# Kernel tuning notes

Measured on AMD Instinct MI355X. Metric: run time of the kernel, lower is better.

## Reference

```python
import jax, jax.numpy as jnp
import numpy as np

N = 50000   # nodes
E = 400000  # edges
D = 128     # hidden = out dim
H = 4       # heads
DH = 32     # head dim (D // H)
T = 3       # node types
R = 6       # relation (edge) types
L = 2       # layers
EPS = 1e-5


def setup_inputs() -> dict:
    key = jax.random.key(0)
    ks = jax.random.split(key, 12)
    s = D ** -0.5
    sh = DH ** -0.5
    return {
        "h": jax.random.normal(ks[0], (N, D), jnp.float32),
        "src": jax.random.randint(ks[1], (E,), 0, N),
        "dst": jax.random.randint(ks[2], (E,), 0, N),
        "ntype": jnp.sort(jax.random.randint(ks[3], (N,), 0, T)),
        "etype": jnp.sort(jax.random.randint(ks[4], (E,), 0, R)),
        # per-layer HGTConv params (stacked over L)
        "Wk": jax.random.normal(ks[5], (L, T, D, D), jnp.float32) * s,
        "Wq": jax.random.normal(ks[6], (L, T, D, D), jnp.float32) * s,
        "Wv": jax.random.normal(ks[7], (L, T, D, D), jnp.float32) * s,
        "Wa": jax.random.normal(ks[8], (L, T, D, D), jnp.float32) * s,
        "W_att": jax.random.normal(ks[9], (L, H, R, DH, DH), jnp.float32) * sh,
        "W_msg": jax.random.normal(ks[10], (L, H, R, DH, DH), jnp.float32) * sh,
        "pri": jnp.ones((L, H, R), jnp.float32),
        "skip": jnp.ones((L, T), jnp.float32),
        "ln_g": jnp.ones((L, D), jnp.float32),
        "ln_b": jnp.zeros((L, D), jnp.float32),
        # LayerAggregator params
        "agg_w": jnp.ones((L,), jnp.float32),
        "agg_g": jnp.ones((D,), jnp.float32),
        "agg_b": jnp.zeros((D,), jnp.float32),
    }


def typed_linear(x, types, W):
    # W: [T, in, out]; per-node-type linear (DGL TypedLinear, no bias)
    out = x @ W[0]
    for t in range(1, W.shape[0]):
        out = jnp.where((types == t)[:, None], x @ W[t], out)
    return out


def edge_typed(x, etype, W):
    # x: [E, H, DH]; W: [H, R, DH, DH]; per-relation, per-head linear
    out = jnp.einsum('ehd,hdo->eho', x, W[:, 0])
    for r in range(1, W.shape[1]):
        out = jnp.where((etype == r)[:, None, None],
                        jnp.einsum('ehd,hdo->eho', x, W[:, r]), out)
    return out


def layer_norm(x, g, b):
    mu = x.mean(-1, keepdims=True)
    var = ((x - mu) ** 2).mean(-1, keepdims=True)
    return (x - mu) * jax.lax.rsqrt(var + EPS) * g + b


def hgt_layer(x, src, dst, ntype, etype, Wk, Wq, Wv, Wa, W_att, W_msg, pri, skip):
    n = x.shape[0]
    k = typed_linear(x, ntype, Wk).reshape(n, H, DH)
    q = typed_linear(x, ntype, Wq).reshape(n, H, DH)
    v = typed_linear(x, ntype, Wv).reshape(n, H, DH)
    kw = edge_typed(k[src], etype, W_att)          # [E,H,DH]
    mv = edge_typed(v[src], etype, W_msg)          # [E,H,DH]
    a = (kw * q[dst]).sum(-1) * pri.T[etype] / np.sqrt(DH).astype(np.float32)  # [E,H]
    # edge softmax over destination nodes
    mx = jax.lax.stop_gradient(jax.ops.segment_max(a, dst, num_segments=n))
    ex = jnp.exp(a - mx[dst])
    den = jax.ops.segment_sum(ex, dst, num_segments=n)
    att = ex / den[dst]                             # [E,H]
    agg = jax.ops.segment_sum(att[:, :, None] * mv, dst, num_segments=n)
    h_a = typed_linear(agg.reshape(n, H * DH), ntype, Wa)
    sk = jax.nn.sigmoid(skip)[ntype][:, None]
    return h_a * sk + x * (1.0 - sk)                # skip gate (dropout = eval identity)


def reference(h, src, dst, ntype, etype, Wk, Wq, Wv, Wa, W_att, W_msg,
              pri, skip, ln_g, ln_b, agg_w, agg_g, agg_b):
    x = h
    outs = []
    for l in range(L):
        ho = hgt_layer(x, src, dst, ntype, etype, Wk[l], Wq[l], Wv[l], Wa[l],
                       W_att[l], W_msg[l], pri[l], skip[l])
        # residual is Identity (in_dim == out_dim), dropout is eval-mode identity
        x = layer_norm(x + ho, ln_g[l], ln_b[l])
        outs.append(x)
    w = jax.nn.softmax(agg_w)
    mixed = sum(w[i] * outs[i] for i in range(L))
    return layer_norm(mixed, agg_g, agg_b)  # [N, D]; per-type dict is just slicing by ntype
```

## Files before the change

kernel.cpp:

```cpp
#include <hip/hip_runtime.h>

#define NN 50000
#define NE 400000
#define DD 128
#define HH 4
#define DHH 32
#define TT 3
#define RR 6
#define LL 2
#define EPSF 1e-5f

typedef unsigned short ushort_t;
typedef unsigned int uint_t;
typedef __attribute__((ext_vector_type(8))) short short8_t;
typedef __attribute__((ext_vector_type(4))) float float4_t;

__device__ inline ushort_t f2bf(float f){
  union { float f; uint_t u; } x; x.f = f;
  uint_t r = x.u + 0x7fffu + ((x.u >> 16) & 1u);
  return (ushort_t)(r >> 16);
}
__device__ inline float bf2f(ushort_t u){
  union { uint_t u; float f; } x; x.u = ((uint_t)u) << 16;
  return x.f;
}
__device__ inline uint_t pack2(float a, float b){
  return (uint_t)f2bf(a) | ((uint_t)f2bf(b) << 16);
}

__global__ void hist_kernel(const int* __restrict__ dst, int* __restrict__ cnt){
  int e = blockIdx.x*256 + threadIdx.x;
  if (e < NE) atomicAdd(&cnt[dst[e]], 1);
}

__global__ void scan_kernel(const int* __restrict__ deg, int* __restrict__ rowptr){
  __shared__ int wsum[16];
  __shared__ int carrySh;
  int tid = threadIdx.x, lane = tid & 63, w = tid >> 6;
  if (tid == 0){ carrySh = 0; rowptr[0] = 0; }
  __syncthreads();
  for (int base = 0; base < NN; base += 1024){
    int i = base + tid;
    int v = (i < NN) ? deg[i] : 0;
    int s = v;
    #pragma unroll
    for (int off=1; off<64; off<<=1){ int t = __shfl_up(s, off); if (lane >= off) s += t; }
    if (lane == 63) wsum[w] = s;
    __syncthreads();
    if (w == 0 && lane < 16){
      int t = wsum[lane];
      #pragma unroll
      for (int off=1; off<16; off<<=1){ int u = __shfl_up(t, off); if (lane >= off) t += u; }
      wsum[lane] = t;
    }
    __syncthreads();
    int waveOff = (w == 0) ? 0 : wsum[w-1];
    int incl = s + waveOff + carrySh;
    if (i < NN) rowptr[i+1] = incl;
    __syncthreads();
    if (tid == 0) carrySh += wsum[15];
    __syncthreads();
  }
}

__global__ void scatter_kernel(const int* __restrict__ dst, const int* __restrict__ src,
                               const int* __restrict__ etype, const int* __restrict__ rowptr,
                               int* __restrict__ cnt, uint_t* __restrict__ sr){
  int e = blockIdx.x*256 + threadIdx.x;
  if (e < NE){
    int d = dst[e];
    int pos = rowptr[d] + atomicAdd(&cnt[d], 1);
    sr[pos] = (uint_t)src[e] | ((uint_t)etype[e] << 27);
  }
}

__global__ void wprep_kernel(const float* __restrict__ Wk, const float* __restrict__ Wq,
                             const float* __restrict__ Wv, const float* __restrict__ Wa,
                             ushort_t* __restrict__ Wkf, ushort_t* __restrict__ Wqf,
                             ushort_t* __restrict__ Wvf, ushort_t* __restrict__ Waf){
  int i = blockIdx.x*256 + threadIdx.x;
  if (i < TT*DD*DD){
    int j = i & 7, m = (i>>3)&15, kg = (i>>7)&3, ks = (i>>9)&3, tile = (i>>11)&7, t = i>>14;
    int d = ks*32 + kg*4 + (j&3) + ((j>>2)<<4);
    int o = tile*16 + m;
    size_t srcI = (size_t)t*16384 + (size_t)d*DD + o;
    Wkf[i] = f2bf(Wk[srcI]);
    Wqf[i] = f2bf(Wq[srcI]);
    Wvf[i] = f2bf(Wv[srcI]);
    Waf[i] = f2bf(Wa[srcI]);
  }
}

__global__ void wprep2_kernel(const float* __restrict__ Watt, const float* __restrict__ Wmsg,
                              ushort_t* __restrict__ Wattf, ushort_t* __restrict__ Wmsgf){
  int i = blockIdx.x*256 + threadIdx.x;
  if (i < HH*RR*DHH*DHH){
    int j = i & 7, m = (i>>3)&15, kg = (i>>7)&3;
    int tile = (i>>9) % 12, h = i / 6144;
    int nout = tile*16 + m;
    int r = nout >> 5, dd = nout & 31;
    int k = kg*4 + (j&3) + ((j>>2)<<4);
    Wattf[i] = f2bf(Watt[(((h*RR + r)*DHH + dd)<<5) + k]);
    Wmsgf[i] = f2bf(Wmsg[(((h*RR + r)*DHH + k)<<5) + dd]);
  }
}

__global__ __launch_bounds__(256) void kqv_kernel(
    const float* __restrict__ x, const int* __restrict__ ntype,
    const float* __restrict__ Wk, const float* __restrict__ Wq, const float* __restrict__ Wv,
    const ushort_t* __restrict__ Wkf, const ushort_t* __restrict__ Wqf, const ushort_t* __restrict__ Wvf,
    const ushort_t* __restrict__ Wattf, const ushort_t* __restrict__ Wmsgf,
    const float* __restrict__ pri,
    ushort_t* __restrict__ kout, ushort_t* __restrict__ qh, ushort_t* __restrict__ vhat)
{
  __shared__ int nts[16];
  __shared__ ushort_t smem[24704];
  ushort_t* xs_ = smem;
  ushort_t* qs_ = smem + 2112;
  ushort_t* vs_ = smem + 4224;
  ushort_t* ks_ = smem + 6336;
  ushort_t* stg1 = smem;
  ushort_t* stg2 = smem + 12352;
  int tid = threadIdx.x;
  int n0 = blockIdx.x * 16;
  if (tid < 16) nts[tid] = ntype[n0 + tid];
  #pragma unroll
  for (int it=0; it<8; it++){
    int i = tid + it*256;
    xs_[(i>>7)*132 + (i&127)] = f2bf(x[(size_t)n0*DD + i]);
  }
  __syncthreads();
  int t0 = nts[0];
  bool uni = true;
  #pragma unroll
  for (int j=1;j<16;j++) uni = uni && (nts[j] == t0);

  int lane = tid & 63;
  union U8 { struct { uint2 lo, hi; } u; short8_t s; uint4 q; };

  if (uni){
    int w = tid >> 6;
    int m = lane & 15, kg = lane >> 4;
    float4_t acck0{0.f,0.f,0.f,0.f}, acck1{0.f,0.f,0.f,0.f};
    float4_t accq0{0.f,0.f,0.f,0.f}, accq1{0.f,0.f,0.f,0.f};
    float4_t accv0{0.f,0.f,0.f,0.f}, accv1{0.f,0.f,0.f,0.f};
    const ushort_t* wkf = Wkf + (size_t)t0*16384;
    const ushort_t* wqf = Wqf + (size_t)t0*16384;
    const ushort_t* wvf = Wvf + (size_t)t0*16384;
    int tA = 2*w, tB = 2*w+1;
    #pragma unroll
    for (int ks=0; ks<4; ks++){
      U8 a_;
      a_.u.lo = *(const uint2*)&xs_[m*132 + ks*32 + kg*4];
      a_.u.hi = *(const uint2*)&xs_[m*132 + ks*32 + kg*4 + 16];
      int offA = (((tA*4 + ks)*4 + kg) << 7) + (m << 3);
      int offB = (((tB*4 + ks)*4 + kg) << 7) + (m << 3);
      U8 bk0, bk1, bq0, bq1, bv0, bv1;
      bk0.q = *(const uint4*)(wkf + offA);
      bk1.q = *(const uint4*)(wkf + offB);
      bq0.q = *(const uint4*)(wqf + offA);
      bq1.q = *(const uint4*)(wqf + offB);
      bv0.q = *(const uint4*)(wvf + offA);
      bv1.q = *(const uint4*)(wvf + offB);
      acck0 = __builtin_amdgcn_mfma_f32_16x16x32_bf16(bk0.s, a_.s, acck0, 0,0,0);
      acck1 = __builtin_amdgcn_mfma_f32_16x16x32_bf16(bk1.s, a_.s, acck1, 0,0,0);
      accq0 = __builtin_amdgcn_mfma_f32_16x16x32_bf16(bq0.s, a_.s, accq0, 0,0,0);
      accq1 = __builtin_amdgcn_mfma_f32_16x16x32_bf16(bq1.s, a_.s, accq1, 0,0,0);
      accv0 = __builtin_amdgcn_mfma_f32_16x16x32_bf16(bv0.s, a_.s, accv0, 0,0,0);
      accv1 = __builtin_amdgcn_mfma_f32_16x16x32_bf16(bv1.s, a_.s, accv1, 0,0,0);
    }
    int cA = tA*16 + (kg<<2), cB = tB*16 + (kg<<2);
    *(uint2*)(&ks_[m*132 + cA]) = make_uint2(pack2(acck0[0],acck0[1]), pack2(acck0[2],acck0[3]));
    *(uint2*)(&ks_[m*132 + cB]) = make_uint2(pack2(acck1[0],acck1[1]), pack2(acck1[2],acck1[3]));
    *(uint2*)(&qs_[m*132 + cA]) = make_uint2(pack2(accq0[0],accq0[1]), pack2(accq0[2],accq0[3]));
    *(uint2*)(&qs_[m*132 + cB]) = make_uint2(pack2(accq1[0],accq1[1]), pack2(accq1[2],accq1[3]));
    *(uint2*)(&vs_[m*132 + cA]) = make_uint2(pack2(accv0[0],accv0[1]), pack2(accv0[2],accv0[3]));
    *(uint2*)(&vs_[m*132 + cB]) = make_uint2(pack2(accv1[0],accv1[1]), pack2(accv1[2],accv1[3]));
  } else {
    int c = tid & 127, nb = (tid >> 7) * 8;
    float ak[8], aq[8], av[8];
    #pragma unroll
    for (int j=0;j<8;j++){ ak[j]=0.f; aq[j]=0.f; av[j]=0.f; }
    #pragma unroll
    for (int j=0;j<8;j++){
      int t = nts[nb+j];
      const float* wk = Wk + (size_t)t*DD*DD + c;
      const float* wq = Wq + (size_t)t*DD*DD + c;
      const float* wv = Wv + (size_t)t*DD*DD + c;
      float sk=0.f, sq=0.f, sv=0.f;
      for (int d=0; d<DD; d++){
        float xv = bf2f(xs_[(nb+j)*132 + d]);
        sk += xv*wk[d*DD];
        sq += xv*wq[d*DD];
        sv += xv*wv[d*DD];
      }
      ak[j]=sk; aq[j]=sq; av[j]=sv;
    }
    #pragma unroll
    for (int j=0;j<8;j++){
      ks_[(nb+j)*132 + c]=f2bf(ak[j]);
      qs_[(nb+j)*132 + c]=f2bf(aq[j]);
      vs_[(nb+j)*132 + c]=f2bf(av[j]);
    }
  }
  __syncthreads();

  int h = tid >> 6;
  int m = lane & 15, kg = lane >> 4;
  U8 aq_, av_;
  aq_.u.lo = *(const uint2*)&qs_[m*132 + (h<<5) + (kg<<2)];
  aq_.u.hi = *(const uint2*)&qs_[m*132 + (h<<5) + (kg<<2) + 16];
  av_.u.lo = *(const uint2*)&vs_[m*132 + (h<<5) + (kg<<2)];
  av_.u.hi = *(const uint2*)&vs_[m*132 + (h<<5) + (kg<<2) + 16];
  {
    int row = tid >> 4, coff = (tid & 15) * 8;
    uint4 kv4;
    kv4.x = *(const uint_t*)&ks_[row*132 + coff];
    kv4.y = *(const uint_t*)&ks_[row*132 + coff + 2];
    kv4.z = *(const uint_t*)&ks_[row*132 + coff + 4];
    kv4.w = *(const uint_t*)&ks_[row*132 + coff + 6];
    *(uint4*)(kout + (size_t)(n0+row)*DD + coff) = kv4;
  }
  __syncthreads();

  const ushort_t* wqb = Wattf + h*(RR*DHH*DHH);
  const ushort_t* wvb = Wmsgf + h*(RR*DHH*DHH);

  #pragma unroll
  for (int nt=0; nt<12; nt++){
    int frag = ((nt*4 + kg)<<7) + (m<<3);
    U8 bq_;
    bq_.q = *(const uint4*)(wqb + frag);
    float4_t accq{0.f,0.f,0.f,0.f};
    accq = __builtin_amdgcn_mfma_f32_16x16x32_bf16(bq_.s, aq_.s, accq, 0,0,0);
    int nout0 = nt*16 + (kg<<2);
    int r = nout0 >> 5, dd0 = nout0 & 31;
    float scale = pri[h*RR + r] * 0.17677669529663687f;
    *(uint2*)(&stg1[m*772 + r*DD + (h<<5) + dd0]) =
        make_uint2(pack2(accq[0]*scale, accq[1]*scale), pack2(accq[2]*scale, accq[3]*scale));
  }
  __syncthreads();

  #pragma unroll
  for (int it=0; it<6; it++){
    int idx = tid + it*256;
    int row = idx / 96;
    int off = (idx - row*96) * 8;
    uint4 q4;
    q4.x = *(const uint_t*)&stg1[row*772 + off];
    q4.y = *(const uint_t*)&stg1[row*772 + off + 2];
    q4.z = *(const uint_t*)&stg1[row*772 + off + 4];
    q4.w = *(const uint_t*)&stg1[row*772 + off + 6];
    *(uint4*)(qh + (size_t)(n0+row)*768 + off) = q4;
  }
  #pragma unroll
  for (int nt=0; nt<12; nt++){
    int frag = ((nt*4 + kg)<<7) + (m<<3);
    U8 bv_;
    bv_.q = *(const uint4*)(wvb + frag);
    float4_t accv{0.f,0.f,0.f,0.f};
    accv = __builtin_amdgcn_mfma_f32_16x16x32_bf16(bv_.s, av_.s, accv, 0,0,0);
    int nout0 = nt*16 + (kg<<2);
    int r = nout0 >> 5, dd0 = nout0 & 31;
    *(uint2*)(&stg2[m*772 + r*DD + (h<<5) + dd0]) =
        make_uint2(pack2(accv[0],accv[1]), pack2(accv[2],accv[3]));
  }
  __syncthreads();

  #pragma unroll
  for (int it=0; it<6; it++){
    int idx = tid + it*256;
    int row = idx / 96;
    int off = (idx - row*96) * 8;
    uint4 v4;
    v4.x = *(const uint_t*)&stg2[row*772 + off];
    v4.y = *(const uint_t*)&stg2[row*772 + off + 2];
    v4.z = *(const uint_t*)&stg2[row*772 + off + 4];
    v4.w = *(const uint_t*)&stg2[row*772 + off + 6];
    *(uint4*)(vhat + (size_t)(n0+row)*768 + off) = v4;
  }
}

__global__ __launch_bounds__(256) void reduce_kernel(
    const ushort_t* __restrict__ kb, const ushort_t* __restrict__ qh,
    const ushort_t* __restrict__ vhat,
    const int* __restrict__ rowptr, const uint_t* __restrict__ src_r,
    ushort_t* __restrict__ agg16)
{
  int n = blockIdx.x*4 + (threadIdx.x >> 6);
  if (n >= NN) return;
  int lane = threadIdx.x & 63;
  int b = rowptr[n], e1 = rowptr[n+1];
  const uint_t* qbase = (const uint_t*)(qh + (size_t)n*RR*DD) + lane;
  uint_t qn0 = qbase[0*64], qn1 = qbase[1*64], qn2 = qbase[2*64];
  uint_t qn3 = qbase[3*64], qn4 = qbase[4*64], qn5 = qbase[5*64];
  float m = -1e30f, den = 0.f, ac0 = 0.f, ac1 = 0.f;
  for (int i=b; i<e1; i+=8){
    int m8 = e1 - i; if (m8 > 8) m8 = 8;
    uint_t sr8[8];
    #pragma unroll
    for (int jj=0;jj<8;jj++) sr8[jj] = src_r[i + ((jj < m8) ? jj : (m8-1))];
    uint_t kk8[8], vv8[8];
    #pragma unroll
    for (int jj=0;jj<8;jj++){
      uint_t sr_ = sr8[jj];
      size_t s = (size_t)(sr_ & 0x07FFFFFFu);
      kk8[jj] = *(const uint_t*)(kb + s*DD + (lane<<1));
      vv8[jj] = *(const uint_t*)(vhat + (s*RR + (sr_>>27))*DD + (lane<<1));
    }
    float p8[8];
    #pragma unroll
    for (int jj=0;jj<8;jj++){
      int r = (int)(sr8[jj] >> 27);
      uint_t qw = qn0;
      qw = (r==1) ? qn1 : qw;
      qw = (r==2) ? qn2 : qw;
      qw = (r==3) ? qn3 : qw;
      qw = (r==4) ? qn4 : qw;
      qw = (r==5) ? qn5 : qw;
      uint_t kw = kk8[jj];
      float pp = bf2f((ushort_t)(kw & 0xffffu))*bf2f((ushort_t)(qw & 0xffffu))
               + bf2f((ushort_t)(kw >> 16))   *bf2f((ushort_t)(qw >> 16));
      #pragma unroll
      for (int off=1; off<16; off<<=1) pp += __shfl_xor(pp, off);
      p8[jj] = (jj < m8) ? pp : -1e30f;
    }
    float mb = p8[0];
    #pragma unroll
    for (int jj=1;jj<8;jj++) mb = fmaxf(mb, p8[jj]);
    float mnew = fmaxf(m, mb);
    float corr = __expf(m - mnew);
    den *= corr; ac0 *= corr; ac1 *= corr;
    m = mnew;
    #pragma unroll
    for (int jj=0;jj<8;jj++){
      float ex = __expf(p8[jj] - m);
      den += ex;
      ac0 += ex * bf2f((ushort_t)(vv8[jj] & 0xffffu));
      ac1 += ex * bf2f((ushort_t)(vv8[jj] >> 16));
    }
  }
  float inv = (den > 0.f) ? 1.f/den : 0.f;
  uint_t packed = (uint_t)f2bf(ac0*inv) | ((uint_t)f2bf(ac1*inv) << 16);
  *(uint_t*)(agg16 + (size_t)n*DD + (lane<<1)) = packed;
}

__global__ __launch_bounds__(256) void ha_kernel(
    const ushort_t* __restrict__ agg16, const float* __restrict__ x, const int* __restrict__ ntype,
    const float* __restrict__ Wa, const ushort_t* __restrict__ Waf, const float* __restrict__ skipl,
    const float* __restrict__ lng, const float* __restrict__ lnb,
    float* __restrict__ xout)
{
  __shared__ ushort_t as[16][132];
  __shared__ float xs[16][132];
  __shared__ int nts[16];
  int tid = threadIdx.x;
  int n0 = blockIdx.x * 16;
  {
    int row = tid >> 4, col = (tid & 15) * 8;
    uint4 t4 = *(const uint4*)(agg16 + (size_t)(n0+row)*DD + col);
    *(uint2*)&as[row][col]   = make_uint2(t4.x, t4.y);
    *(uint2*)&as[row][col+4] = make_uint2(t4.z, t4.w);
  }
  if (tid < 16) nts[tid] = ntype[n0 + tid];
  __syncthreads();
  int t0 = nts[0];
  bool uni = true;
  #pragma unroll
  for (int j=1;j<16;j++) uni = uni && (nts[j] == t0);

  if (uni){
    int lane = tid & 63, w = tid >> 6;
    int m = lane & 15, kg = lane >> 4;
    float4_t acc0{0.f,0.f,0.f,0.f}, acc1{0.f,0.f,0.f,0.f};
    const ushort_t* waf = Waf + (size_t)t0*16384;
    int tA = 2*w, tB = 2*w+1;
    union U8 { struct { uint2 lo, hi; } u; short8_t s; uint4 q; };
    #pragma unroll
    for (int ks=0; ks<4; ks++){
      U8 a_;
      a_.u.lo = *(const uint2*)&as[m][ks*32 + kg*4];
      a_.u.hi = *(const uint2*)&as[m][ks*32 + kg*4 + 16];
      U8 b0, b1;
      b0.q = *(const uint4*)(waf + ((((tA*4 + ks)*4 + kg) << 7) + (m << 3)));
      b1.q = *(const uint4*)(waf + ((((tB*4 + ks)*4 + kg) << 7) + (m << 3)));
      acc0 = __builtin_amdgcn_mfma_f32_16x16x32_bf16(b0.s, a_.s, acc0, 0,0,0);
      acc1 = __builtin_amdgcn_mfma_f32_16x16x32_bf16(b1.s, a_.s, acc1, 0,0,0);
    }
    float sk = 1.f/(1.f + __expf(-skipl[t0]));
    int cA = tA*16 + (kg<<2), cB = tB*16 + (kg<<2);
    #pragma unroll
    for (int i=0;i<4;i++){
      float xva = x[(size_t)(n0+m)*DD + cA + i];
      float xvb = x[(size_t)(n0+m)*DD + cB + i];
      xs[m][cA+i] = acc0[i]*sk + xva*(2.f - sk);
      xs[m][cB+i] = acc1[i]*sk + xvb*(2.f - sk);
    }
  } else {
    int c = tid & 127, nb = (tid >> 7) * 8;
    float acc[8];
    #pragma unroll
    for (int j=0;j<8;j++) acc[j]=0.f;
    #pragma unroll
    for (int j=0;j<8;j++){
      int t = nts[nb+j];
      const float* wa = Wa + (size_t)t*DD*DD + c;
      float sacc2 = 0.f;
      for (int d=0; d<DD; d++)
        sacc2 += bf2f(as[nb+j][d]) * wa[d*DD];
      acc[j] = sacc2;
    }
    #pragma unroll
    for (int j=0;j<8;j++){
      int n = n0 + nb + j;
      float sk2 = 1.f/(1.f + __expf(-skipl[nts[nb+j]]));
      float xv = x[(size_t)n*DD + c];
      xs[nb+j][c] = acc[j]*sk2 + xv*(2.f - sk2);
    }
  }
  __syncthreads();
  int lane = tid & 63;
  int r0 = tid >> 6;
  #pragma unroll
  for (int rr = r0; rr < 16; rr += 4){
    float t0v = xs[rr][lane], t1v = xs[rr][lane+64];
    float s = t0v + t1v;
    #pragma unroll
    for (int off=32; off>0; off>>=1) s += __shfl_xor(s, off);
    float mu = s * (1.f/DD);
    float d0 = t0v-mu, d1 = t1v-mu;
    float vs = d0*d0 + d1*d1;
    #pragma unroll
    for (int off=32; off>0; off>>=1) vs += __shfl_xor(vs, off);
    float inv = rsqrtf(vs*(1.f/DD) + EPSF);
    size_t base = (size_t)(n0+rr)*DD;
    xout[base+lane]    = d0*inv*lng[lane]    + lnb[lane];
    xout[base+lane+64] = d1*inv*lng[lane+64] + lnb[lane+64];
  }
}

__global__ __launch_bounds__(256) void final_kernel(
    const float* __restrict__ x1, const float* __restrict__ x2,
    const float* __restrict__ aggw, const float* __restrict__ g, const float* __restrict__ b,
    float* __restrict__ out)
{
  int lane = threadIdx.x & 63;
  int n = blockIdx.x*4 + (threadIdx.x >> 6);
  float a0 = aggw[0], a1 = aggw[1];
  float m = fmaxf(a0, a1);
  float e0 = __expf(a0-m), e1 = __expf(a1-m);
  float inv01 = 1.f/(e0+e1);
  float w0 = e0*inv01, w1 = e1*inv01;
  size_t base = (size_t)n*DD;
  float t0 = w0*x1[base+lane]    + w1*x2[base+lane];
  float t1 = w0*x1[base+lane+64] + w1*x2[base+lane+64];
  float s = t0 + t1;
  #pragma unroll
  for (int off=32; off>0; off>>=1) s += __shfl_xor(s, off);
  float mu = s * (1.f/DD);
  float d0 = t0-mu, d1 = t1-mu;
  float vs = d0*d0 + d1*d1;
  #pragma unroll
  for (int off=32; off>0; off>>=1) vs += __shfl_xor(vs, off);
  float invv = rsqrtf(vs*(1.f/DD) + EPSF);
  out[base+lane]    = d0*invv*g[lane]    + b[lane];
  out[base+lane+64] = d1*invv*g[lane+64] + b[lane+64];
}

extern "C" void kernel_launch(void* const* d_in, const int* in_sizes, int n_in,
                              void* d_out, int out_size, void* d_ws, size_t ws_size,
                              hipStream_t stream)
{
  (void)in_sizes; (void)n_in; (void)out_size; (void)ws_size;
  const float* h_in  = (const float*)d_in[0];
  const int*   src   = (const int*)d_in[1];
  const int*   dst   = (const int*)d_in[2];
  const int*   ntype = (const int*)d_in[3];
  const int*   etype = (const int*)d_in[4];
  const float* Wk    = (const float*)d_in[5];
  const float* Wq    = (const float*)d_in[6];
  const float* Wv    = (const float*)d_in[7];
  const float* Wa    = (const float*)d_in[8];
  const float* Watt  = (const float*)d_in[9];
  const float* Wmsg  = (const float*)d_in[10];
  const float* pri   = (const float*)d_in[11];
  const float* skp   = (const float*)d_in[12];
  const float* lng   = (const float*)d_in[13];
  const float* lnb   = (const float*)d_in[14];
  const float* aggw  = (const float*)d_in[15];
  const float* aggg  = (const float*)d_in[16];
  const float* aggb_ = (const float*)d_in[17];

  size_t P = (size_t)NN*DD;
  ushort_t* kb16 = (ushort_t*)d_ws;
  ushort_t* qh   = kb16 + P;
  ushort_t* vhat = qh + (size_t)NN*RR*DD;
  ushort_t* agg16 = vhat + (size_t)NN*RR*DD;
  float* out0  = (float*)(agg16 + P);
  int* rowptr = (int*)(out0 + P);
  int* cnt    = rowptr + NN + 1;
  uint_t* srcr = (uint_t*)(cnt + NN);
  ushort_t* wkF = (ushort_t*)(srcr + NE);
  ushort_t* wqF = wkF + (size_t)TT*DD*DD;
  ushort_t* wvF = wqF + (size_t)TT*DD*DD;
  ushort_t* waF = wvF + (size_t)TT*DD*DD;
  ushort_t* wattF = waF + (size_t)TT*DD*DD;
  ushort_t* wmsgF = wattF + (size_t)HH*RR*DHH*DHH;
  float* xout = (float*)d_out;

  hipMemsetAsync(cnt, 0, NN*sizeof(int), stream);
  hist_kernel<<<(NE+255)/256, 256, 0, stream>>>(dst, cnt);
  scan_kernel<<<1, 1024, 0, stream>>>(cnt, rowptr);
  hipMemsetAsync(cnt, 0, NN*sizeof(int), stream);
  scatter_kernel<<<(NE+255)/256, 256, 0, stream>>>(dst, src, etype, rowptr, cnt, srcr);

  const float* x = h_in;
  for (int l=0; l<LL; l++){
    const float* Wk_l  = Wk  + (size_t)l*TT*DD*DD;
    const float* Wq_l  = Wq  + (size_t)l*TT*DD*DD;
    const float* Wv_l  = Wv  + (size_t)l*TT*DD*DD;
    const float* Wa_l  = Wa  + (size_t)l*TT*DD*DD;
    const float* Wat_l = Watt + (size_t)l*HH*RR*DHH*DHH;
    const float* Wms_l = Wmsg + (size_t)l*HH*RR*DHH*DHH;
    const float* pri_l = pri + (size_t)l*HH*RR;
    const float* skp_l = skp + (size_t)l*TT;

    wprep_kernel<<<(TT*DD*DD+255)/256, 256, 0, stream>>>(Wk_l, Wq_l, Wv_l, Wa_l,
                                                         wkF, wqF, wvF, waF);
    wprep2_kernel<<<(HH*RR*DHH*DHH+255)/256, 256, 0, stream>>>(Wat_l, Wms_l, wattF, wmsgF);
    kqv_kernel<<<NN/16, 256, 0, stream>>>(x, ntype, Wk_l, Wq_l, Wv_l, wkF, wqF, wvF,
                                          wattF, wmsgF, pri_l, kb16, qh, vhat);
    reduce_kernel<<<(NN+3)/4, 256, 0, stream>>>(kb16, qh, vhat, rowptr, srcr, agg16);
    float* xo = (l == 0) ? out0 : xout;
    ha_kernel<<<NN/16, 256, 0, stream>>>(agg16, x, ntype, Wa_l, waF, skp_l,
                                         lng + (size_t)l*DD, lnb + (size_t)l*DD, xo);
    x = xo;
  }
  final_kernel<<<NN/4, 256, 0, stream>>>(out0, xout, aggw, aggg, aggb_, xout);
}
```

Before: 427.3 us.

## Fuse final aggregation into last layer, merge weight prep, chunk scan

Three changes are made. The scan kernel moves from a loop of 1024-wide block scans with several barriers per step to a per-thread chunk sum, followed by one block scan and a serial local prefix. The two weight-prep kernels become one launch. The final layer-mix LayerNorm is folded into the last layer's ha_kernel epilogue, which removes a kernel launch and a full read/write pass over the node features. The chunked scan reads deg strided by thread, so its loads are uncoalesced.

```diff
diff --git a/kernel.cpp b/kernel.cpp
--- a/kernel.cpp
+++ b/kernel.cpp
@@ -33,33 +33,35 @@
   if (e < NE) atomicAdd(&cnt[dst[e]], 1);
 }
 
-__global__ void scan_kernel(const int* __restrict__ deg, int* __restrict__ rowptr){
+__global__ __launch_bounds__(1024) void scan_kernel(const int* __restrict__ deg,
+                                                    int* __restrict__ rowptr){
   __shared__ int wsum[16];
-  __shared__ int carrySh;
   int tid = threadIdx.x, lane = tid & 63, w = tid >> 6;
-  if (tid == 0){ carrySh = 0; rowptr[0] = 0; }
-  __syncthreads();
-  for (int base = 0; base < NN; base += 1024){
-    int i = base + tid;
-    int v = (i < NN) ? deg[i] : 0;
-    int s = v;
-    #pragma unroll
-    for (int off=1; off<64; off<<=1){ int t = __shfl_up(s, off); if (lane >= off) s += t; }
-    if (lane == 63) wsum[w] = s;
-    __syncthreads();
-    if (w == 0 && lane < 16){
-      int t = wsum[lane];
-      #pragma unroll
-      for (int off=1; off<16; off<<=1){ int u = __shfl_up(t, off); if (lane >= off) t += u; }
-      wsum[lane] = t;
-    }
-    __syncthreads();
-    int waveOff = (w == 0) ? 0 : wsum[w-1];
-    int incl = s + waveOff + carrySh;
-    if (i < NN) rowptr[i+1] = incl;
-    __syncthreads();
-    if (tid == 0) carrySh += wsum[15];
-    __syncthreads();
+  const int CH = 49;
+  int base = tid * CH;
+  int tot = 0;
+  for (int j=0;j<CH;j++){
+    int i = base + j;
+    tot += (i < NN) ? deg[i] : 0;
+  }
+  int s = tot;
+  #pragma unroll
+  for (int off=1; off<64; off<<=1){ int t = __shfl_up(s, off); if (lane >= off) s += t; }
+  if (lane == 63) wsum[w] = s;
+  __syncthreads();
+  if (w == 0 && lane < 16){
+    int t = wsum[lane];
+    #pragma unroll
+    for (int off=1; off<16; off<<=1){ int u = __shfl_up(t, off); if (lane >= off) t += u; }
+    wsum[lane] = t;
+  }
+  __syncthreads();
+  int waveOff = (w == 0) ? 0 : wsum[w-1];
+  int run = (s - tot) + waveOff;
+  if (tid == 0) rowptr[0] = 0;
+  for (int j=0;j<CH;j++){
+    int i = base + j;
+    if (i < NN){ run += deg[i]; rowptr[i+1] = run; }
   }
 }
 
@@ -76,8 +78,10 @@
 
 __global__ void wprep_kernel(const float* __restrict__ Wk, const float* __restrict__ Wq,
                              const float* __restrict__ Wv, const float* __restrict__ Wa,
+                             const float* __restrict__ Watt, const float* __restrict__ Wmsg,
                              ushort_t* __restrict__ Wkf, ushort_t* __restrict__ Wqf,
-                             ushort_t* __restrict__ Wvf, ushort_t* __restrict__ Waf){
+                             ushort_t* __restrict__ Wvf, ushort_t* __restrict__ Waf,
+                             ushort_t* __restrict__ Wattf, ushort_t* __restrict__ Wmsgf){
   int i = blockIdx.x*256 + threadIdx.x;
   if (i < TT*DD*DD){
     int j = i & 7, m = (i>>3)&15, kg = (i>>7)&3, ks = (i>>9)&3, tile = (i>>11)&7, t = i>>14;
@@ -89,11 +93,6 @@
     Wvf[i] = f2bf(Wv[srcI]);
     Waf[i] = f2bf(Wa[srcI]);
   }
-}
-
-__global__ void wprep2_kernel(const float* __restrict__ Watt, const float* __restrict__ Wmsg,
-                              ushort_t* __restrict__ Wattf, ushort_t* __restrict__ Wmsgf){
-  int i = blockIdx.x*256 + threadIdx.x;
   if (i < HH*RR*DHH*DHH){
     int j = i & 7, m = (i>>3)&15, kg = (i>>7)&3;
     int tile = (i>>9) % 12, h = i / 6144;
@@ -349,6 +348,8 @@
     const ushort_t* __restrict__ agg16, const float* __restrict__ x, const int* __restrict__ ntype,
     const float* __restrict__ Wa, const ushort_t* __restrict__ Waf, const float* __restrict__ skipl,
     const float* __restrict__ lng, const float* __restrict__ lnb,
+    const float* __restrict__ out0p, const float* __restrict__ aggw,
+    const float* __restrict__ fg, const float* __restrict__ fb, int isFinal,
     float* __restrict__ xout)
 {
   __shared__ ushort_t as[16][132];
@@ -434,37 +435,32 @@
     for (int off=32; off>0; off>>=1) vs += __shfl_xor(vs, off);
     float inv = rsqrtf(vs*(1.f/DD) + EPSF);
     size_t base = (size_t)(n0+rr)*DD;
-    xout[base+lane]    = d0*inv*lng[lane]    + lnb[lane];
-    xout[base+lane+64] = d1*inv*lng[lane+64] + lnb[lane+64];
-  }
-}
-
-__global__ __launch_bounds__(256) void final_kernel(
-    const float* __restrict__ x1, const float* __restrict__ x2,
-    const float* __restrict__ aggw, const float* __restrict__ g, const float* __restrict__ b,
-    float* __restrict__ out)
-{
-  int lane = threadIdx.x & 63;
-  int n = blockIdx.x*4 + (threadIdx.x >> 6);
-  float a0 = aggw[0], a1 = aggw[1];
-  float m = fmaxf(a0, a1);
-  float e0 = __expf(a0-m), e1 = __expf(a1-m);
-  float inv01 = 1.f/(e0+e1);
-  float w0 = e0*inv01, w1 = e1*inv01;
-  size_t base = (size_t)n*DD;
-  float t0 = w0*x1[base+lane]    + w1*x2[base+lane];
-  float t1 = w0*x1[base+lane+64] + w1*x2[base+lane+64];
-  float s = t0 + t1;
-  #pragma unroll
-  for (int off=32; off>0; off>>=1) s += __shfl_xor(s, off);
-  float mu = s * (1.f/DD);
-  float d0 = t0-mu, d1 = t1-mu;
-  float vs = d0*d0 + d1*d1;
-  #pragma unroll
-  for (int off=32; off>0; off>>=1) vs += __shfl_xor(vs, off);
-  float invv = rsqrtf(vs*(1.f/DD) + EPSF);
-  out[base+lane]    = d0*invv*g[lane]    + b[lane];
-  out[base+lane+64] = d1*invv*g[lane+64] + b[lane+64];
+    float z0 = d0*inv*lng[lane]    + lnb[lane];
+    float z1 = d1*inv*lng[lane+64] + lnb[lane+64];
+    if (!isFinal){
+      xout[base+lane]    = z0;
+      xout[base+lane+64] = z1;
+    } else {
+      float a0 = aggw[0], a1 = aggw[1];
+      float mm = fmaxf(a0, a1);
+      float e0 = __expf(a0-mm), e1 = __expf(a1-mm);
+      float i01 = 1.f/(e0+e1);
+      float w0 = e0*i01, w1 = e1*i01;
+      float u0 = w0*out0p[base+lane]    + w1*z0;
+      float u1 = w0*out0p[base+lane+64] + w1*z1;
+      float ss = u0 + u1;
+      #pragma unroll
+      for (int off=32; off>0; off>>=1) ss += __shfl_xor(ss, off);
+      float mu2 = ss * (1.f/DD);
+      float f0 = u0-mu2, f1 = u1-mu2;
+      float vs2 = f0*f0 + f1*f1;
+      #pragma unroll
+      for (int off=32; off>0; off>>=1) vs2 += __shfl_xor(vs2, off);
+      float inv2 = rsqrtf(vs2*(1.f/DD) + EPSF);
+      xout[base+lane]    = f0*inv2*fg[lane]    + fb[lane];
+      xout[base+lane+64] = f1*inv2*fg[lane+64] + fb[lane+64];
+    }
+  }
 }
 
 extern "C" void kernel_launch(void* const* d_in, const int* in_sizes, int n_in,
@@ -525,16 +521,15 @@
     const float* pri_l = pri + (size_t)l*HH*RR;
     const float* skp_l = skp + (size_t)l*TT;
 
-    wprep_kernel<<<(TT*DD*DD+255)/256, 256, 0, stream>>>(Wk_l, Wq_l, Wv_l, Wa_l,
-                                                         wkF, wqF, wvF, waF);
-    wprep2_kernel<<<(HH*RR*DHH*DHH+255)/256, 256, 0, stream>>>(Wat_l, Wms_l, wattF, wmsgF);
+    wprep_kernel<<<(TT*DD*DD+255)/256, 256, 0, stream>>>(Wk_l, Wq_l, Wv_l, Wa_l, Wat_l, Wms_l,
+                                                         wkF, wqF, wvF, waF, wattF, wmsgF);
     kqv_kernel<<<NN/16, 256, 0, stream>>>(x, ntype, Wk_l, Wq_l, Wv_l, wkF, wqF, wvF,
                                           wattF, wmsgF, pri_l, kb16, qh, vhat);
     reduce_kernel<<<(NN+3)/4, 256, 0, stream>>>(kb16, qh, vhat, rowptr, srcr, agg16);
     float* xo = (l == 0) ? out0 : xout;
     ha_kernel<<<NN/16, 256, 0, stream>>>(agg16, x, ntype, Wa_l, waF, skp_l,
-                                         lng + (size_t)l*DD, lnb + (size_t)l*DD, xo);
+                                         lng + (size_t)l*DD, lnb + (size_t)l*DD,
+                                         out0, aggw, aggg, aggb_, (l == LL-1) ? 1 : 0, xo);
     x = xo;
   }
-  final_kernel<<<NN/4, 256, 0, stream>>>(out0, xout, aggw, aggg, aggb_, xout);
-}
+}
```

New measurement: 477.0 us. +11.6%, slower.
